# Kernel optimization log

Hardware: AMD Instinct MI355X
Metric: run time of the kernel (lower is better)

Reference implementation:

```python
import jax, jax.numpy as jnp
import numpy as np

NUM_RADIAL = 16
HIDDEN = 128
OUT_DIM = 128
N_LAYERS = 3
N_NODES = 20000
N_EDGES = 640000


def _orthogonal(key, rows, cols):
    # mimic nn.init.orthogonal_ for a [rows, cols] weight
    n = max(rows, cols)
    a = jax.random.normal(key, (n, min(rows, cols)), dtype=jnp.float32)
    q, r = jnp.linalg.qr(a)
    q = q * jnp.sign(jnp.diagonal(r))  # make deterministic-ish sign
    w = q[:rows, :cols] if rows >= cols else q[:cols, :rows].T
    return w.astype(jnp.float32)


def setup_inputs() -> dict:
    key = jax.random.key(0)
    ks = jax.random.split(key, 8)
    distance_representation = jax.random.normal(ks[0], (N_EDGES, NUM_RADIAL), dtype=jnp.float32)
    message = jax.random.normal(ks[1], (N_EDGES, HIDDEN), dtype=jnp.float32)
    edge_index = jax.random.randint(ks[2], (2, N_EDGES), 0, N_NODES, dtype=jnp.int32)
    # parameters (torch Linear stores weight as [out, in])
    Wd = _orthogonal(ks[3], HIDDEN, NUM_RADIAL)          # linear_distance.weight
    layer_keys = jax.random.split(ks[4], N_LAYERS)
    Ws = jnp.stack([_orthogonal(k, HIDDEN, HIDDEN) for k in layer_keys])  # [L, H, H]
    bs = jnp.zeros((N_LAYERS, HIDDEN), dtype=jnp.float32)
    Wout = _orthogonal(ks[5], OUT_DIM, HIDDEN)           # linear_out.weight
    return {
        "distance_representation": distance_representation,
        "message": message,
        "edge_index": edge_index,
        "num_nodes": N_NODES,
        "Wd": Wd,
        "Ws": Ws,
        "bs": bs,
        "Wout": Wout,
    }


def reference(distance_representation, message, edge_index, num_nodes, Wd, Ws, bs, Wout):
    # distance gate: [E, NUM_RADIAL] @ Wd.T -> [E, H]
    gate = distance_representation @ Wd.T
    transformed_message = gate * message                 # [E, H]
    target_index = edge_index[1]
    # edge -> node scatter-add aggregation
    node_embedding = jax.ops.segment_sum(
        transformed_message, target_index, num_segments=num_nodes)  # [N, H]
    for i in range(Ws.shape[0]):
        node_embedding = jax.nn.silu(node_embedding @ Ws[i].T + bs[i])
    return node_embedding @ Wout.T                       # [N, OUT_DIM]
```

## Files before the change

kernel.cpp:

```cpp
#include <hip/hip_runtime.h>

#define HID 128
#define NR  16
#define NLAYER 4
#define CHUNK 16

__device__ __forceinline__ float dot4f(float4 a, float4 b) {
    return a.x * b.x + a.y * b.y + a.z * b.z + a.w * b.w;
}

__global__ void hist_kernel(const int* __restrict__ eidx, int* __restrict__ hist, int E) {
    int i = (blockIdx.x * blockDim.x + threadIdx.x) * 4;
    if (i + 4 <= E) {
        int4 v = *(const int4*)(eidx + E + i);
        atomicAdd(&hist[v.x], 1);
        atomicAdd(&hist[v.y], 1);
        atomicAdd(&hist[v.z], 1);
        atomicAdd(&hist[v.w], 1);
    } else {
        for (; i < E; ++i) atomicAdd(&hist[eidx[E + i]], 1);
    }
}

__global__ __launch_bounds__(1024) void scan_kernel(const int* __restrict__ hist,
                                                    int* __restrict__ curs, int N) {
    __shared__ int part[1024];
    const int tid = threadIdx.x;
    const int per = (N + 1023) >> 10;
    const int base = tid * per;
    int s = 0;
    for (int i = 0; i < per; ++i) {
        int idx = base + i;
        if (idx < N) s += hist[idx];
    }
    part[tid] = s;
    __syncthreads();
    for (int off = 1; off < 1024; off <<= 1) {
        int v = part[tid];
        int add = (tid >= off) ? part[tid - off] : 0;
        __syncthreads();
        part[tid] = v + add;
        __syncthreads();
    }
    int run = (tid > 0) ? part[tid - 1] : 0;
    for (int i = 0; i < per; ++i) {
        int idx = base + i;
        if (idx < N) {
            curs[idx] = run;
            run += hist[idx];
        }
    }
}

__global__ void scatter_kernel(const int* __restrict__ eidx, int* __restrict__ curs,
                               int* __restrict__ sorted, int* __restrict__ stgt, int E) {
    int i = (blockIdx.x * blockDim.x + threadIdx.x) * 4;
    if (i + 4 <= E) {
        int4 v = *(const int4*)(eidx + E + i);
        int p;
        p = atomicAdd(&curs[v.x], 1); sorted[p] = i + 0; stgt[p] = v.x;
        p = atomicAdd(&curs[v.y], 1); sorted[p] = i + 1; stgt[p] = v.y;
        p = atomicAdd(&curs[v.z], 1); sorted[p] = i + 2; stgt[p] = v.z;
        p = atomicAdd(&curs[v.w], 1); sorted[p] = i + 3; stgt[p] = v.w;
    } else {
        for (; i < E; ++i) {
            int t = eidx[E + i];
            int p = atomicAdd(&curs[t], 1);
            sorted[p] = i; stgt[p] = t;
        }
    }
}

__global__ void transpose_kernel(const float* __restrict__ Ws, const float* __restrict__ Wout,
                                 float* __restrict__ WT) {
    int i = blockIdx.x * blockDim.x + threadIdx.x;
    if (i >= NLAYER * HID * HID) return;
    int l = i >> 14;
    int rem = i & 16383;
    int h = rem >> 7, k = rem & 127;
    const float* src = (l < 3) ? (Ws + ((size_t)l << 14)) : Wout;
    WT[((size_t)l << 14) + (size_t)k * HID + h] = src[(size_t)h * HID + k];
}

__global__ __launch_bounds__(256, 4) void gather_kernel(
    const float* __restrict__ dist, const float* __restrict__ msg,
    const float* __restrict__ Wd, const int* __restrict__ sorted,
    const int* __restrict__ stgt, float* __restrict__ node_emb, int E)
{
    __shared__ float sdist[4][CHUNK * NR];

    const int tid  = threadIdx.x;
    const int lane = tid & 63;
    const int wv   = tid >> 6;
    const long base = ((long)blockIdx.x * 4 + wv) * CHUNK;
    if (base >= E) return;
    const int cnt = (E - base < CHUNK) ? (int)(E - base) : CHUNK;

    float4 wd0[4], wd1[4];
#pragma unroll
    for (int q = 0; q < 4; ++q) {
        wd0[q] = *(const float4*)(Wd + (size_t)(2 * lane)     * NR + q * 4);
        wd1[q] = *(const float4*)(Wd + (size_t)(2 * lane + 1) * NR + q * 4);
    }

    int ids[CHUNK], tg[CHUNK];
    if (cnt == CHUNK) {
#pragma unroll
        for (int q = 0; q < CHUNK / 4; ++q) {
            int4 a = *(const int4*)(sorted + base + q * 4);
            int4 b = *(const int4*)(stgt   + base + q * 4);
            ids[q*4+0] = a.x; ids[q*4+1] = a.y; ids[q*4+2] = a.z; ids[q*4+3] = a.w;
            tg [q*4+0] = b.x; tg [q*4+1] = b.y; tg [q*4+2] = b.z; tg [q*4+3] = b.w;
        }
    } else {
#pragma unroll
        for (int i = 0; i < CHUNK; ++i) {
            ids[i] = (i < cnt) ? sorted[base + i] : 0;
            tg[i]  = (i < cnt) ? stgt[base + i]  : -1;
        }
    }

    float dv[CHUNK / 4];
#pragma unroll
    for (int g = 0; g < CHUNK / 4; ++g) {
        int e = ids[g * 4 + (lane >> 4)];
        dv[g] = dist[(size_t)e * NR + (lane & 15)];
    }

    float2 m[CHUNK];
#pragma unroll
    for (int i = 0; i < CHUNK; ++i)
        m[i] = *(const float2*)(msg + (size_t)ids[i] * HID + 2 * lane);

    float* sd = sdist[wv];
#pragma unroll
    for (int g = 0; g < CHUNK / 4; ++g)
        sd[g * 64 + lane] = dv[g];

    float a0 = 0.f, a1 = 0.f;
#pragma unroll
    for (int i = 0; i < CHUNK; ++i) {
        if (i < cnt) {
            const float4* dr = (const float4*)(sd + i * NR);
            float4 d0 = dr[0], d1 = dr[1], d2 = dr[2], d3 = dr[3];
            float g0 = dot4f(d0, wd0[0]) + dot4f(d1, wd0[1]) +
                       dot4f(d2, wd0[2]) + dot4f(d3, wd0[3]);
            float g1 = dot4f(d0, wd1[0]) + dot4f(d1, wd1[1]) +
                       dot4f(d2, wd1[2]) + dot4f(d3, wd1[3]);
            a0 += g0 * m[i].x;
            a1 += g1 * m[i].y;
            bool fl = (i == cnt - 1) || (tg[i + 1] != tg[i]);
            if (fl) {
                float* dst = node_emb + (size_t)tg[i] * HID + 2 * lane;
                unsafeAtomicAdd(dst,     a0);
                unsafeAtomicAdd(dst + 1, a1);
                a0 = 0.f; a1 = 0.f;
            }
        }
    }
}

__global__ __launch_bounds__(512) void mlp_kernel(
    float* __restrict__ data, const float* __restrict__ WT,
    const float* __restrict__ bs, int N)
{
    __shared__ float xa[64][132];

    const int tid = threadIdx.x;
    const int nb  = blockIdx.x * 64;
    const int hq  = tid & 31, h0 = hq * 4;
    const int nq  = tid >> 5, n0 = nq * 4;

    for (int i = tid; i < 64 * 32; i += 512) {
        int n = i >> 5, kq = i & 31;
        float4 v = make_float4(0.f, 0.f, 0.f, 0.f);
        if (nb + n < N) v = *(const float4*)(data + (size_t)(nb + n) * HID + kq * 4);
        *(float4*)(&xa[n][kq * 4]) = v;
    }
    __syncthreads();

    for (int l = 0; l < NLAYER; ++l) {
        const float* __restrict__ W = WT + ((size_t)l << 14);
        float acc[4][4];
        if (l < 3) {
            float b[4];
#pragma unroll
            for (int j = 0; j < 4; ++j) b[j] = bs[l * HID + h0 + j];
#pragma unroll
            for (int i = 0; i < 4; ++i)
#pragma unroll
                for (int j = 0; j < 4; ++j) acc[i][j] = b[j];
        } else {
#pragma unroll
            for (int i = 0; i < 4; ++i)
#pragma unroll
                for (int j = 0; j < 4; ++j) acc[i][j] = 0.f;
        }

        for (int k4 = 0; k4 < 32; ++k4) {
            float4 xv[4];
#pragma unroll
            for (int i = 0; i < 4; ++i) xv[i] = *(const float4*)(&xa[n0 + i][k4 * 4]);
            float4 wr[4];
#pragma unroll
            for (int kk = 0; kk < 4; ++kk)
                wr[kk] = *(const float4*)(W + (size_t)(k4 * 4 + kk) * HID + h0);
#pragma unroll
            for (int i = 0; i < 4; ++i) {
                acc[i][0] += xv[i].x * wr[0].x + xv[i].y * wr[1].x + xv[i].z * wr[2].x + xv[i].w * wr[3].x;
                acc[i][1] += xv[i].x * wr[0].y + xv[i].y * wr[1].y + xv[i].z * wr[2].y + xv[i].w * wr[3].y;
                acc[i][2] += xv[i].x * wr[0].z + xv[i].y * wr[1].z + xv[i].z * wr[2].z + xv[i].w * wr[3].z;
                acc[i][3] += xv[i].x * wr[0].w + xv[i].y * wr[1].w + xv[i].z * wr[2].w + xv[i].w * wr[3].w;
            }
        }
        __syncthreads();

        if (l < 3) {
#pragma unroll
            for (int i = 0; i < 4; ++i) {
                float4 y;
                y.x = acc[i][0] / (1.f + __expf(-acc[i][0]));
                y.y = acc[i][1] / (1.f + __expf(-acc[i][1]));
                y.z = acc[i][2] / (1.f + __expf(-acc[i][2]));
                y.w = acc[i][3] / (1.f + __expf(-acc[i][3]));
                *(float4*)(&xa[n0 + i][h0]) = y;
            }
            __syncthreads();
        } else {
#pragma unroll
            for (int i = 0; i < 4; ++i) {
                if (nb + n0 + i < N) {
                    float4 y = make_float4(acc[i][0], acc[i][1], acc[i][2], acc[i][3]);
                    *(float4*)(data + (size_t)(nb + n0 + i) * HID + h0) = y;
                }
            }
        }
    }
}

extern "C" void kernel_launch(void* const* d_in, const int* in_sizes, int n_in,
                              void* d_out, int out_size, void* d_ws, size_t ws_size,
                              hipStream_t stream) {
    const float* dist = (const float*)d_in[0];
    const float* msg  = (const float*)d_in[1];
    const int*   eidx = (const int*)d_in[2];
    const float* Wd   = (const float*)d_in[4];
    const float* Ws   = (const float*)d_in[5];
    const float* bs   = (const float*)d_in[6];
    const float* Wout = (const float*)d_in[7];
    float* out = (float*)d_out;

    const int E = in_sizes[1] / HID;
    const int N = out_size / HID;

    int*   hist   = (int*)d_ws;
    int*   curs   = hist + N;
    int*   sorted = curs + N;
    int*   stgt   = sorted + E;
    size_t wt_off = ((size_t)(2 * N + 2 * E) + 3) & ~(size_t)3;
    float* WT     = (float*)d_ws + wt_off;

    hipMemsetAsync(hist, 0, (size_t)N * sizeof(int), stream);
    hipMemsetAsync(out, 0, (size_t)N * HID * sizeof(float), stream);

    const int qE = (E + 3) / 4;
    hist_kernel   <<<(qE + 255) / 256, 256, 0, stream>>>(eidx, hist, E);
    scan_kernel   <<<1, 1024, 0, stream>>>(hist, curs, N);
    scatter_kernel<<<(qE + 255) / 256, 256, 0, stream>>>(eidx, curs, sorted, stgt, E);
    transpose_kernel<<<(NLAYER * HID * HID + 255) / 256, 256, 0, stream>>>(Ws, Wout, WT);

    const long waves = ((long)E + CHUNK - 1) / CHUNK;
    gather_kernel <<<(int)((waves + 3) / 4), 256, 0, stream>>>(dist, msg, Wd, sorted, stgt, out, E);
    mlp_kernel    <<<(N + 63) / 64, 512, 0, stream>>>(out, WT, bs, N);
}
```

Before: 304.6 us.

## Fuse transpose into scan, pack sorted index pairs, split gate dot across lanes

Folds the weight transpose into the scan launch as extra blocks and stages the histogram in LDS for the scan, removing one kernel launch. Scatter now writes (edge id, target) as one int2 so gather loads both with a single vector load. In the gather kernel each lane computes half of the 16-wide radial dot product for four channels and exchanges partial sums with its neighbour via a shuffle, halving the Wd registers and LDS reads per lane. This costs an extra shuffle and selects per edge, plus a large static LDS allocation in the prep kernel that every block reserves, including the transpose blocks.

Measured after the change: 290.8 us. -4.5%, faster.

```diff
diff --git a/kernel.cpp b/kernel.cpp
--- a/kernel.cpp
+++ b/kernel.cpp
@@ -4,6 +4,7 @@
 #define NR  16
 #define NLAYER 4
 #define CHUNK 16
+#define MAXN_LDS 20480
 
 __device__ __forceinline__ float dot4f(float4 a, float4 b) {
     return a.x * b.x + a.y * b.y + a.z * b.z + a.w * b.w;
@@ -22,16 +23,36 @@
     }
 }
 
-__global__ __launch_bounds__(1024) void scan_kernel(const int* __restrict__ hist,
-                                                    int* __restrict__ curs, int N) {
+__global__ __launch_bounds__(1024) void prep_kernel(const int* __restrict__ hist,
+                                                    int* __restrict__ curs, int N,
+                                                    const float* __restrict__ Ws,
+                                                    const float* __restrict__ Wout,
+                                                    float* __restrict__ WT) {
+    const int tid = threadIdx.x;
+    if (blockIdx.x > 0) {
+        int idx = (blockIdx.x - 1) * 1024 + tid;
+        if (idx < NLAYER * HID * HID) {
+            int l = idx >> 14;
+            int rem = idx & 16383;
+            int h = rem >> 7, k = rem & 127;
+            const float* src = (l < 3) ? (Ws + ((size_t)l << 14)) : Wout;
+            WT[((size_t)l << 14) + (size_t)k * HID + h] = src[(size_t)h * HID + k];
+        }
+        return;
+    }
+    __shared__ int sh[MAXN_LDS];
     __shared__ int part[1024];
-    const int tid = threadIdx.x;
+    const bool use_lds = (N <= MAXN_LDS);
+    if (use_lds) {
+        for (int i = tid; i < N; i += 1024) sh[i] = hist[i];
+        __syncthreads();
+    }
     const int per = (N + 1023) >> 10;
     const int base = tid * per;
     int s = 0;
     for (int i = 0; i < per; ++i) {
         int idx = base + i;
-        if (idx < N) s += hist[idx];
+        if (idx < N) s += use_lds ? sh[idx] : hist[idx];
     }
     part[tid] = s;
     __syncthreads();
@@ -47,45 +68,34 @@
         int idx = base + i;
         if (idx < N) {
             curs[idx] = run;
-            run += hist[idx];
+            run += use_lds ? sh[idx] : hist[idx];
         }
     }
 }
 
 __global__ void scatter_kernel(const int* __restrict__ eidx, int* __restrict__ curs,
-                               int* __restrict__ sorted, int* __restrict__ stgt, int E) {
+                               int2* __restrict__ pairs, int E) {
     int i = (blockIdx.x * blockDim.x + threadIdx.x) * 4;
     if (i + 4 <= E) {
         int4 v = *(const int4*)(eidx + E + i);
         int p;
-        p = atomicAdd(&curs[v.x], 1); sorted[p] = i + 0; stgt[p] = v.x;
-        p = atomicAdd(&curs[v.y], 1); sorted[p] = i + 1; stgt[p] = v.y;
-        p = atomicAdd(&curs[v.z], 1); sorted[p] = i + 2; stgt[p] = v.z;
-        p = atomicAdd(&curs[v.w], 1); sorted[p] = i + 3; stgt[p] = v.w;
+        p = atomicAdd(&curs[v.x], 1); pairs[p] = make_int2(i + 0, v.x);
+        p = atomicAdd(&curs[v.y], 1); pairs[p] = make_int2(i + 1, v.y);
+        p = atomicAdd(&curs[v.z], 1); pairs[p] = make_int2(i + 2, v.z);
+        p = atomicAdd(&curs[v.w], 1); pairs[p] = make_int2(i + 3, v.w);
     } else {
         for (; i < E; ++i) {
             int t = eidx[E + i];
             int p = atomicAdd(&curs[t], 1);
-            sorted[p] = i; stgt[p] = t;
-        }
-    }
-}
-
-__global__ void transpose_kernel(const float* __restrict__ Ws, const float* __restrict__ Wout,
-                                 float* __restrict__ WT) {
-    int i = blockIdx.x * blockDim.x + threadIdx.x;
-    if (i >= NLAYER * HID * HID) return;
-    int l = i >> 14;
-    int rem = i & 16383;
-    int h = rem >> 7, k = rem & 127;
-    const float* src = (l < 3) ? (Ws + ((size_t)l << 14)) : Wout;
-    WT[((size_t)l << 14) + (size_t)k * HID + h] = src[(size_t)h * HID + k];
+            pairs[p] = make_int2(i, t);
+        }
+    }
 }
 
 __global__ __launch_bounds__(256, 4) void gather_kernel(
     const float* __restrict__ dist, const float* __restrict__ msg,
-    const float* __restrict__ Wd, const int* __restrict__ sorted,
-    const int* __restrict__ stgt, float* __restrict__ node_emb, int E)
+    const float* __restrict__ Wd, const int2* __restrict__ pairs,
+    float* __restrict__ node_emb, int E)
 {
     __shared__ float sdist[4][CHUNK * NR];
 
@@ -96,27 +106,28 @@
     if (base >= E) return;
     const int cnt = (E - base < CHUNK) ? (int)(E - base) : CHUNK;
 
-    float4 wd0[4], wd1[4];
-#pragma unroll
-    for (int q = 0; q < 4; ++q) {
-        wd0[q] = *(const float4*)(Wd + (size_t)(2 * lane)     * NR + q * 4);
-        wd1[q] = *(const float4*)(Wd + (size_t)(2 * lane + 1) * NR + q * 4);
+    const int base_ch = (lane >> 1) << 2;
+    const int kh      = (lane & 1) * 8;
+    float4 wdh[4][2];
+#pragma unroll
+    for (int j = 0; j < 4; ++j) {
+        wdh[j][0] = *(const float4*)(Wd + (size_t)(base_ch + j) * NR + kh);
+        wdh[j][1] = *(const float4*)(Wd + (size_t)(base_ch + j) * NR + kh + 4);
     }
 
     int ids[CHUNK], tg[CHUNK];
     if (cnt == CHUNK) {
 #pragma unroll
-        for (int q = 0; q < CHUNK / 4; ++q) {
-            int4 a = *(const int4*)(sorted + base + q * 4);
-            int4 b = *(const int4*)(stgt   + base + q * 4);
-            ids[q*4+0] = a.x; ids[q*4+1] = a.y; ids[q*4+2] = a.z; ids[q*4+3] = a.w;
-            tg [q*4+0] = b.x; tg [q*4+1] = b.y; tg [q*4+2] = b.z; tg [q*4+3] = b.w;
+        for (int q = 0; q < CHUNK / 2; ++q) {
+            int4 v = *(const int4*)(pairs + base + q * 2);
+            ids[q*2+0] = v.x; tg[q*2+0] = v.y;
+            ids[q*2+1] = v.z; tg[q*2+1] = v.w;
         }
     } else {
 #pragma unroll
         for (int i = 0; i < CHUNK; ++i) {
-            ids[i] = (i < cnt) ? sorted[base + i] : 0;
-            tg[i]  = (i < cnt) ? stgt[base + i]  : -1;
+            int2 v = (i < cnt) ? pairs[base + i] : make_int2(0, -1);
+            ids[i] = v.x; tg[i] = v.y;
         }
     }
 
@@ -137,16 +148,23 @@
     for (int g = 0; g < CHUNK / 4; ++g)
         sd[g * 64 + lane] = dv[g];
 
+    const bool odd = (lane & 1);
     float a0 = 0.f, a1 = 0.f;
 #pragma unroll
     for (int i = 0; i < CHUNK; ++i) {
         if (i < cnt) {
-            const float4* dr = (const float4*)(sd + i * NR);
-            float4 d0 = dr[0], d1 = dr[1], d2 = dr[2], d3 = dr[3];
-            float g0 = dot4f(d0, wd0[0]) + dot4f(d1, wd0[1]) +
-                       dot4f(d2, wd0[2]) + dot4f(d3, wd0[3]);
-            float g1 = dot4f(d0, wd1[0]) + dot4f(d1, wd1[1]) +
-                       dot4f(d2, wd1[2]) + dot4f(d3, wd1[3]);
+            const float4* dr = (const float4*)(sd + i * NR + kh);
+            float4 d0 = dr[0], d1 = dr[1];
+            float p0 = dot4f(d0, wdh[0][0]) + dot4f(d1, wdh[0][1]);
+            float p1 = dot4f(d0, wdh[1][0]) + dot4f(d1, wdh[1][1]);
+            float p2 = dot4f(d0, wdh[2][0]) + dot4f(d1, wdh[2][1]);
+            float p3 = dot4f(d0, wdh[3][0]) + dot4f(d1, wdh[3][1]);
+            float s0 = odd ? p0 : p2;
+            float s1 = odd ? p1 : p3;
+            float r0 = __shfl_xor(s0, 1, 64);
+            float r1 = __shfl_xor(s1, 1, 64);
+            float g0 = (odd ? p2 : p0) + r0;
+            float g1 = (odd ? p3 : p1) + r1;
             a0 += g0 * m[i].x;
             a1 += g1 * m[i].y;
             bool fl = (i == cnt - 1) || (tg[i + 1] != tg[i]);
@@ -255,21 +273,21 @@
 
     int*   hist   = (int*)d_ws;
     int*   curs   = hist + N;
-    int*   sorted = curs + N;
-    int*   stgt   = sorted + E;
-    size_t wt_off = ((size_t)(2 * N + 2 * E) + 3) & ~(size_t)3;
+    size_t pr_off = ((size_t)(2 * N) + 3) & ~(size_t)3;
+    int2*  pairs  = (int2*)((int*)d_ws + pr_off);
+    size_t wt_off = (pr_off + (size_t)2 * E + 3) & ~(size_t)3;
     float* WT     = (float*)d_ws + wt_off;
 
     hipMemsetAsync(hist, 0, (size_t)N * sizeof(int), stream);
     hipMemsetAsync(out, 0, (size_t)N * HID * sizeof(float), stream);
 
     const int qE = (E + 3) / 4;
+    const int tblocks = (NLAYER * HID * HID + 1023) / 1024;
     hist_kernel   <<<(qE + 255) / 256, 256, 0, stream>>>(eidx, hist, E);
-    scan_kernel   <<<1, 1024, 0, stream>>>(hist, curs, N);
-    scatter_kernel<<<(qE + 255) / 256, 256, 0, stream>>>(eidx, curs, sorted, stgt, E);
-    transpose_kernel<<<(NLAYER * HID * HID + 255) / 256, 256, 0, stream>>>(Ws, Wout, WT);
+    prep_kernel   <<<1 + tblocks, 1024, 0, stream>>>(hist, curs, N, Ws, Wout, WT);
+    scatter_kernel<<<(qE + 255) / 256, 256, 0, stream>>>(eidx, curs, pairs, E);
 
     const long waves = ((long)E + CHUNK - 1) / CHUNK;
-    gather_kernel <<<(int)((waves + 3) / 4), 256, 0, stream>>>(dist, msg, Wd, sorted, stgt, out, E);
+    gather_kernel <<<(int)((waves + 3) / 4), 256, 0, stream>>>(dist, msg, Wd, pairs, out, E);
     mlp_kernel    <<<(N + 63) / 64, 512, 0, stream>>>(out, WT, bs, N);
 }
```
